# Performance work log

Hardware: AMD Instinct MI355X
Metric: run time of the kernel (lower is better)

The kernel has to match this reference:

```python
import jax, jax.numpy as jnp
import numpy as np

DIM = 128
KNN = 16
EPS = 1e-5


def knn_feature(coords, k):
    # coords: [B, K, D]; returns [B, K, k] nearest-neighbor indices (self excluded)
    inner = -2.0 * jnp.einsum('bid,bjd->bij', coords, coords)
    xx = jnp.sum(coords * coords, axis=-1, keepdims=True)  # [B,K,1]
    dist = xx + jnp.swapaxes(xx, 1, 2) + inner  # [B,K,K]
    K = coords.shape[1]
    diag = jnp.eye(K, dtype=bool)[None]
    dist = jnp.where(diag, 1e9, dist)
    _, idx = jax.lax.top_k(-dist, k)  # smallest distances
    return idx


def setup_inputs() -> dict:
    key = jax.random.key(0)
    ks = jax.random.split(key, 10)
    B, K, C = 8, 4096, DIM
    s1 = 1.0 / np.sqrt(2 * C)
    s2 = 1.0 / np.sqrt(C)
    return {
        'x': jax.random.normal(ks[0], (B, K, C), jnp.float32),
        'pos_embed': jax.random.normal(ks[1], (B, K, C), jnp.float32),
        'rel_pos_coords': jax.random.normal(ks[2], (B, K, 3), jnp.float32),
        'gamma': jnp.ones((C,), jnp.float32),
        'beta': jnp.zeros((C,), jnp.float32),
        'W_a1': jax.random.normal(ks[3], (2 * C, C), jnp.float32) * s1,
        'b_a1': jnp.zeros((C,), jnp.float32),
        'W_a2': jax.random.normal(ks[4], (C, 1), jnp.float32) * s2,
        'b_a2': jnp.zeros((1,), jnp.float32),
        'W_f1': jax.random.normal(ks[5], (2 * C, C), jnp.float32) * s1,
        'b_f1': jnp.zeros((C,), jnp.float32),
    }


def reference(x, pos_embed, rel_pos_coords, gamma, beta, W_a1, b_a1, W_a2, b_a2, W_f1, b_f1):
    B, K, C = x.shape
    k_eff = min(KNN, K - 1)
    # Pre-norm LayerNorm + positional embedding
    mu = jnp.mean(x, axis=-1, keepdims=True)
    var = jnp.mean((x - mu) ** 2, axis=-1, keepdims=True)
    x_norm = (x - mu) * jax.lax.rsqrt(var + EPS) * gamma + beta
    xp = x_norm + pos_embed  # [B,K,C]

    idx = knn_feature(rel_pos_coords, k_eff)  # [B,K,k]
    neighbor_feat = jax.vmap(lambda f, i: f[i])(xp, idx)  # [B,K,k,C]
    self_feat = jnp.broadcast_to(xp[:, :, None, :], neighbor_feat.shape)

    attn_in = jnp.concatenate([self_feat, neighbor_feat], axis=-1)  # [B,K,k,2C]
    h = jax.nn.leaky_relu(attn_in @ W_a1 + b_a1, 0.2)
    logits = h @ W_a2 + b_a2  # [B,K,k,1]
    attn = jax.nn.softmax(logits, axis=2)

    feat_in = jnp.concatenate([self_feat, neighbor_feat - self_feat], axis=-1)
    transformed = jax.nn.leaky_relu(feat_in @ W_f1 + b_f1, 0.2)  # [B,K,k,C]

    agg = jnp.sum(attn * transformed, axis=2)  # [B,K,C]
    # DropPath in eval mode is identity
    return agg
```

## Files before the change

kernel.cpp:

```cpp
#include <hip/hip_runtime.h>

#define B_ 8
#define K_ 4096
#define C_ 128
#define KN 16

typedef __attribute__((ext_vector_type(8))) short bf16x8;
typedef __attribute__((ext_vector_type(4))) float f32x4;

__device__ __forceinline__ unsigned short f2bf(float f) {
  unsigned u = __float_as_uint(f);
  unsigned r = (u + 0x7FFFu + ((u >> 16) & 1u)) >> 16;
  return (unsigned short)r;
}
__device__ __forceinline__ float bf2f(unsigned short s) {
  return __uint_as_float(((unsigned)s) << 16);
}

__device__ __forceinline__ float dist_exact(float4 q, float4 c) {
  float dot = __fadd_rn(__fadd_rn(__fmul_rn(q.x, c.x), __fmul_rn(q.y, c.y)),
                        __fmul_rn(q.z, c.z));
  return __fadd_rn(__fadd_rn(q.w, c.w), __fmul_rn(-2.0f, dot));
}
__device__ __forceinline__ float escr2(float qx2, float qy2, float qz2,
                                       float4 c) {
  return fmaf(-qx2, c.x, fmaf(-qy2, c.y, fmaf(-qz2, c.z, c.w)));
}

__global__ __launch_bounds__(256) void k_pre(
    const float* __restrict__ x, const float* __restrict__ pos,
    const float* __restrict__ gamma, const float* __restrict__ beta,
    const float* __restrict__ Wa1, const float* __restrict__ Wf1,
    const float* __restrict__ coords, unsigned short* __restrict__ A,
    unsigned short* __restrict__ WT, float4* __restrict__ cc4) {
  int blk = blockIdx.x;
  if (blk < 8192) {
    int wave = threadIdx.x >> 6;
    int lane = threadIdx.x & 63;
    size_t row = (size_t)blk * 4 + wave;
    const float2* xr = (const float2*)(x + row * C_);
    const float2* pr = (const float2*)(pos + row * C_);
    float2 a = xr[lane];
    float s = a.x + a.y;
#pragma unroll
    for (int o = 1; o < 64; o <<= 1) s += __shfl_xor(s, o);
    float mu = s * (1.0f / 128.0f);
    float dx = a.x - mu, dy = a.y - mu;
    float v = dx * dx + dy * dy;
#pragma unroll
    for (int o = 1; o < 64; o <<= 1) v += __shfl_xor(v, o);
    float rstd = rsqrtf(v * (1.0f / 128.0f) + 1e-5f);
    float2 gm = ((const float2*)gamma)[lane];
    float2 bt = ((const float2*)beta)[lane];
    float2 pp = pr[lane];
    float o0 = dx * rstd * gm.x + bt.x + pp.x;
    float o1 = dy * rstd * gm.y + bt.y + pp.y;
    ushort2 o = make_ushort2(f2bf(o0), f2bf(o1));
    *(ushort2*)(A + row * C_ + 2 * lane) = o;
  } else if (blk < 8320) {
    int i = (blk - 8192) * 256 + threadIdx.x;
    float px = coords[i * 3], py = coords[i * 3 + 1], pz = coords[i * 3 + 2];
    float w = __fadd_rn(__fadd_rn(__fmul_rn(px, px), __fmul_rn(py, py)),
                        __fmul_rn(pz, pz));
    cc4[i] = make_float4(px, py, pz, w);
  } else {
    int i = (blk - 8320) * 256 + threadIdx.x;
    int q = i >> 7;
    int r = i & 127;
    float v;
    if (q < 128)
      v = Wa1[r * 128 + q];
    else if (q < 256)
      v = Wf1[r * 128 + (q - 128)] - Wf1[(128 + r) * 128 + (q - 128)];
    else {
      int c = (q - 256) >> 1;
      if (((q - 256) & 1) == 0)
        v = Wa1[(128 + r) * 128 + c];
      else
        v = Wf1[(128 + r) * 128 + c];
    }
    WT[i] = f2bf(v);
  }
}

__global__ __launch_bounds__(256, 8) void k_knn(const float4* __restrict__ cc4,
                                                int* __restrict__ idx) {
  __shared__ unsigned cbuf[4][4][64];
  __shared__ unsigned scnt[4][4];
  int wave = threadIdx.x >> 6, lane = threadIdx.x & 63;
  int gw = blockIdx.x * 4 + wave;
  int b = gw >> 10;
  int qbase = (gw & 1023) * 4;
  const float4* cb = cc4 + (size_t)b * K_;
  if (lane < 4) scnt[wave][lane] = 0u;
  __asm__ volatile("s_waitcnt lgkmcnt(0)" ::: "memory");
  float4 Q[4];
  float qx2[4], qy2[4], qz2[4];
#pragma unroll
  for (int qq = 0; qq < 4; ++qq) {
    Q[qq] = cb[qbase + qq];
    qx2[qq] = 2.0f * Q[qq].x;
    qy2[qq] = 2.0f * Q[qq].y;
    qz2[qq] = 2.0f * Q[qq].z;
  }

  float m0 = 1e30f, m1 = 1e30f, m2 = 1e30f, m3 = 1e30f;
#pragma unroll 8
  for (int it = 0; it < 48; ++it) {
    float4 c = cb[(it << 6) + lane];
    m0 = fminf(m0, escr2(qx2[0], qy2[0], qz2[0], c));
    m1 = fminf(m1, escr2(qx2[1], qy2[1], qz2[1], c));
    m2 = fminf(m2, escr2(qx2[2], qy2[2], qz2[2], c));
    m3 = fminf(m3, escr2(qx2[3], qy2[3], qz2[3], c));
  }
  float ub[4];
  float mv[4] = {m0, m1, m2, m3};
#pragma unroll
  for (int qq = 0; qq < 4; ++qq) {
    float v = mv[qq];
#pragma unroll
    for (int k = 2; k <= 64; k <<= 1) {
#pragma unroll
      for (int jj = k >> 1; jj >= 1; jj >>= 1) {
        float o = __shfl_xor(v, jj);
        bool amHigh = (lane & jj) != 0;
        bool up = (lane & k) != 0;
        bool gt = v > o;
        bool take = (amHigh ? !gt : gt) ^ up;
        v = take ? o : v;
      }
    }
    ub[qq] = __shfl(v, 16) + 1e-3f;
  }

#pragma unroll 4
  for (int it = 0; it < 64; ++it) {
    int j = (it << 6) + lane;
    float4 c = cb[j];
#pragma unroll
    for (int qq = 0; qq < 4; ++qq) {
      float e = escr2(qx2[qq], qy2[qq], qz2[qq], c);
      if (e <= ub[qq]) {
        unsigned pos = atomicAdd(&scnt[wave][qq], 1u);
        if (pos < 64u) cbuf[wave][qq][pos] = (unsigned)j;
      }
    }
  }
  __asm__ volatile("s_waitcnt lgkmcnt(0)" ::: "memory");

#pragma unroll
  for (int qq = 0; qq < 4; ++qq) {
    unsigned m = scnt[wave][qq];
    m = m < 64u ? m : 64u;
    bool valid = lane < (int)m;
    unsigned ji = valid ? cbuf[wave][qq][lane] : 0u;
    if (valid && ji == (unsigned)(qbase + qq)) valid = false;
    float4 c = cb[ji];
    float dC = valid ? dist_exact(Q[qq], c) : 1e30f;
    int iC = valid ? (int)ji : 0x7fffffff;
#define SORT_STAGE(KV)                                              \
  {                                                                 \
    const int k = (KV);                                             \
    for (int jj = k >> 1; jj >= 1; jj >>= 1) {                      \
      float od = __shfl_xor(dC, jj);                                \
      int oi = __shfl_xor(iC, jj);                                  \
      bool amHigh = (lane & jj) != 0;                               \
      bool up = (lane & k) != 0;                                    \
      bool gt = (dC > od) || (dC == od && iC > oi);                 \
      bool take = (amHigh ? !gt : gt) ^ up;                         \
      dC = take ? od : dC;                                          \
      iC = take ? oi : iC;                                          \
    }                                                               \
  }
    if (m <= 32u) {
      SORT_STAGE(2) SORT_STAGE(4) SORT_STAGE(8) SORT_STAGE(16) SORT_STAGE(32)
    } else {
      SORT_STAGE(2) SORT_STAGE(4) SORT_STAGE(8) SORT_STAGE(16) SORT_STAGE(32)
      SORT_STAGE(64)
    }
#undef SORT_STAGE
    if (lane < KN)
      idx[((size_t)b * K_ + (qbase + qq)) * KN + lane] = iC;
  }
}

__global__ __launch_bounds__(256) void k_gemm_mfma(
    const unsigned short* __restrict__ A, const unsigned short* __restrict__ BT,
    unsigned short* __restrict__ SN) {
  __shared__ char lB[32768];
  int bb = blockIdx.x & 7;
  int rest = blockIdx.x >> 3;
  int mbl = rest >> 2, nb = rest & 3;
  int m0 = bb * 4096 + mbl * 128, n0 = nb * 128;
  int t = threadIdx.x;
  {
    const char* src = (const char*)(BT + (size_t)n0 * 128);
#pragma unroll
    for (int i = 0; i < 8; ++i) {
      int byte = (t + i * 256) * 16;
      int n = byte >> 8;
      int sb = byte ^ ((n & 7) << 4);
      *(float4*)(lB + sb) = *(const float4*)(src + byte);
    }
  }
  __syncthreads();
  int wave = t >> 6, lane = t & 63;
  int wr = wave >> 1, wc = wave & 1;
  int lm = lane & 15, lk = lane >> 4;
  f32x4 z = {0.f, 0.f, 0.f, 0.f};
  f32x4 acc00 = z, acc01 = z, acc02 = z, acc03 = z;
  f32x4 acc10 = z, acc11 = z, acc12 = z, acc13 = z;
  f32x4 acc20 = z, acc21 = z, acc22 = z, acc23 = z;
  f32x4 acc30 = z, acc31 = z, acc32 = z, acc33 = z;
  const char* abase =
      (const char*)A + (size_t)(m0 + wr * 64 + lm) * 256 + lk * 16;
#pragma unroll
  for (int ks = 0; ks < 4; ++ks) {
    bf16x8 af[4], bfr[4];
#pragma unroll
    for (int mt = 0; mt < 4; ++mt)
      af[mt] = *(const bf16x8*)(abase + (size_t)mt * 4096 + ks * 64);
#pragma unroll
    for (int nt = 0; nt < 4; ++nt) {
      int n_local = wc * 64 + nt * 16 + lm;
      int byte = n_local * 256 + ks * 64 + lk * 16;
      byte ^= (n_local & 7) << 4;
      bfr[nt] = *(const bf16x8*)(lB + byte);
    }
    acc00 = __builtin_amdgcn_mfma_f32_16x16x32_bf16(af[0], bfr[0], acc00, 0, 0, 0);
    acc01 = __builtin_amdgcn_mfma_f32_16x16x32_bf16(af[0], bfr[1], acc01, 0, 0, 0);
    acc02 = __builtin_amdgcn_mfma_f32_16x16x32_bf16(af[0], bfr[2], acc02, 0, 0, 0);
    acc03 = __builtin_amdgcn_mfma_f32_16x16x32_bf16(af[0], bfr[3], acc03, 0, 0, 0);
    acc10 = __builtin_amdgcn_mfma_f32_16x16x32_bf16(af[1], bfr[0], acc10, 0, 0, 0);
    acc11 = __builtin_amdgcn_mfma_f32_16x16x32_bf16(af[1], bfr[1], acc11, 0, 0, 0);
    acc12 = __builtin_amdgcn_mfma_f32_16x16x32_bf16(af[1], bfr[2], acc12, 0, 0, 0);
    acc13 = __builtin_amdgcn_mfma_f32_16x16x32_bf16(af[1], bfr[3], acc13, 0, 0, 0);
    acc20 = __builtin_amdgcn_mfma_f32_16x16x32_bf16(af[2], bfr[0], acc20, 0, 0, 0);
    acc21 = __builtin_amdgcn_mfma_f32_16x16x32_bf16(af[2], bfr[1], acc21, 0, 0, 0);
    acc22 = __builtin_amdgcn_mfma_f32_16x16x32_bf16(af[2], bfr[2], acc22, 0, 0, 0);
    acc23 = __builtin_amdgcn_mfma_f32_16x16x32_bf16(af[2], bfr[3], acc23, 0, 0, 0);
    acc30 = __builtin_amdgcn_mfma_f32_16x16x32_bf16(af[3], bfr[0], acc30, 0, 0, 0);
    acc31 = __builtin_amdgcn_mfma_f32_16x16x32_bf16(af[3], bfr[1], acc31, 0, 0, 0);
    acc32 = __builtin_amdgcn_mfma_f32_16x16x32_bf16(af[3], bfr[2], acc32, 0, 0, 0);
    acc33 = __builtin_amdgcn_mfma_f32_16x16x32_bf16(af[3], bfr[3], acc33, 0, 0, 0);
  }
  f32x4 accs[4][4] = {{acc00, acc01, acc02, acc03},
                      {acc10, acc11, acc12, acc13},
                      {acc20, acc21, acc22, acc23},
                      {acc30, acc31, acc32, acc33}};
#pragma unroll
  for (int mt = 0; mt < 4; ++mt) {
#pragma unroll
    for (int nt = 0; nt < 4; ++nt) {
#pragma unroll
      for (int r = 0; r < 4; ++r) {
        int row = m0 + wr * 64 + mt * 16 + lk * 4 + r;
        int col = n0 + wc * 64 + nt * 16 + lm;
        SN[(size_t)row * 512 + col] = f2bf(accs[mt][nt][r]);
      }
    }
  }
}

__global__ __launch_bounds__(256) void k_attn(
    const unsigned short* __restrict__ SN, const int* __restrict__ idx,
    const float* __restrict__ b_a1, const float* __restrict__ b_f1,
    const float* __restrict__ W_a2, const float* __restrict__ b_a2,
    float* __restrict__ out) {
  int wave = threadIdx.x >> 6, lane = threadIdx.x & 63;
  int g = lane >> 4, r = lane & 15;
  int b = blockIdx.x & 7;
  int w = blockIdx.x >> 3;
  size_t gpt = (size_t)b * K_ + w * 4 + wave;
  const unsigned short* sr = SN + gpt * 512;
  bf16x8 sa8 = *(const bf16x8*)(sr + 8 * r);
  bf16x8 sf8 = *(const bf16x8*)(sr + 128 + 8 * r);
  float4 bav0 = *(const float4*)(b_a1 + 8 * r);
  float4 bav1 = *(const float4*)(b_a1 + 8 * r + 4);
  float4 bfv0 = *(const float4*)(b_f1 + 8 * r);
  float4 bfv1 = *(const float4*)(b_f1 + 8 * r + 4);
  float4 w2v0 = *(const float4*)(W_a2 + 8 * r);
  float4 w2v1 = *(const float4*)(W_a2 + 8 * r + 4);
  float sab[8], sfb[8], w2v[8];
  {
    float bav[8] = {bav0.x, bav0.y, bav0.z, bav0.w, bav1.x, bav1.y, bav1.z, bav1.w};
    float bfv[8] = {bfv0.x, bfv0.y, bfv0.z, bfv0.w, bfv1.x, bfv1.y, bfv1.z, bfv1.w};
    float wv[8] = {w2v0.x, w2v0.y, w2v0.z, w2v0.w, w2v1.x, w2v1.y, w2v1.z, w2v1.w};
#pragma unroll
    for (int i = 0; i < 8; ++i) {
      sab[i] = bf2f((unsigned short)sa8[i]) + bav[i];
      sfb[i] = bf2f((unsigned short)sf8[i]) + bfv[i];
      w2v[i] = wv[i];
    }
  }
  float ba2v = b_a2[0];
  int nv = 0;
  if (lane < 16) nv = idx[gpt * 16 + lane];
  float lgl[4];
  float tsv[4][8];
#pragma unroll
  for (int round = 0; round < 4; ++round) {
    int n = __shfl(nv, round * 4 + g);
    const unsigned short* nr =
        SN + ((size_t)b * K_ + n) * 512 + 256 + 16 * r;
    bf16x8 u0 = *(const bf16x8*)(nr);
    bf16x8 u1 = *(const bf16x8*)(nr + 8);
    float dot = 0.0f;
#pragma unroll
    for (int i = 0; i < 4; ++i) {
      float h = sab[i] + bf2f((unsigned short)u0[2 * i]);
      h = h >= 0.0f ? h : 0.2f * h;
      float tv = sfb[i] + bf2f((unsigned short)u0[2 * i + 1]);
      tv = tv >= 0.0f ? tv : 0.2f * tv;
      dot = fmaf(h, w2v[i], dot);
      tsv[round][i] = tv;
    }
#pragma unroll
    for (int i = 0; i < 4; ++i) {
      float h = sab[4 + i] + bf2f((unsigned short)u1[2 * i]);
      h = h >= 0.0f ? h : 0.2f * h;
      float tv = sfb[4 + i] + bf2f((unsigned short)u1[2 * i + 1]);
      tv = tv >= 0.0f ? tv : 0.2f * tv;
      dot = fmaf(h, w2v[4 + i], dot);
      tsv[round][4 + i] = tv;
    }
#pragma unroll
    for (int o = 1; o < 16; o <<= 1) dot += __shfl_xor(dot, o);
    lgl[round] = dot + ba2v;
  }
  float mx = fmaxf(fmaxf(lgl[0], lgl[1]), fmaxf(lgl[2], lgl[3]));
  mx = fmaxf(mx, __shfl_xor(mx, 16));
  mx = fmaxf(mx, __shfl_xor(mx, 32));
  float e[4];
  float s = 0.0f;
#pragma unroll
  for (int round = 0; round < 4; ++round) {
    e[round] = expf(lgl[round] - mx);
    s += e[round];
  }
  s += __shfl_xor(s, 16);
  s += __shfl_xor(s, 32);
  float inv = 1.0f / s;
  float o8[8] = {0, 0, 0, 0, 0, 0, 0, 0};
#pragma unroll
  for (int round = 0; round < 4; ++round) {
    float a = e[round] * inv;
#pragma unroll
    for (int i = 0; i < 8; ++i) o8[i] = fmaf(a, tsv[round][i], o8[i]);
  }
#pragma unroll
  for (int i = 0; i < 8; ++i) {
    o8[i] += __shfl_xor(o8[i], 16);
    o8[i] += __shfl_xor(o8[i], 32);
  }
  if (g == 0) {
    float* op = out + gpt * 128 + 8 * r;
    *(float4*)op = make_float4(o8[0], o8[1], o8[2], o8[3]);
    *(float4*)(op + 4) = make_float4(o8[4], o8[5], o8[6], o8[7]);
  }
}

extern "C" void kernel_launch(void* const* d_in, const int* in_sizes, int n_in,
                              void* d_out, int out_size, void* d_ws,
                              size_t ws_size, hipStream_t stream) {
  const float* x = (const float*)d_in[0];
  const float* pos = (const float*)d_in[1];
  const float* coords = (const float*)d_in[2];
  const float* gamma = (const float*)d_in[3];
  const float* beta = (const float*)d_in[4];
  const float* Wa1 = (const float*)d_in[5];
  const float* ba1 = (const float*)d_in[6];
  const float* Wa2 = (const float*)d_in[7];
  const float* ba2 = (const float*)d_in[8];
  const float* Wf1 = (const float*)d_in[9];
  const float* bf1 = (const float*)d_in[10];
  float* out = (float*)d_out;

  char* ws = (char*)d_ws;
  unsigned short* A = (unsigned short*)ws;
  unsigned short* SN = (unsigned short*)(ws + (size_t)16 * 1024 * 1024);
  unsigned short* WT = (unsigned short*)(ws + (size_t)80 * 1024 * 1024);
  int* idx = (int*)(ws + (size_t)80 * 1024 * 1024 + 512 * 1024);
  float4* cc4 = (float4*)(ws + (size_t)80 * 1024 * 1024 + 2560 * 1024);

  k_pre<<<8576, 256, 0, stream>>>(x, pos, gamma, beta, Wa1, Wf1, coords, A, WT,
                                  cc4);
  k_knn<<<2048, 256, 0, stream>>>(cc4, idx);
  k_gemm_mfma<<<1024, 256, 0, stream>>>(A, WT, SN);
  k_attn<<<8192, 256, 0, stream>>>(SN, idx, ba1, bf1, Wa2, ba2, out);
}
```

Before: 114.5 us.

## Vectorize LayerNorm rows, stage GEMM output through LDS, reduce KNN unroll

```diff
diff --git a/kernel.cpp b/kernel.cpp
--- a/kernel.cpp
+++ b/kernel.cpp
@@ -34,37 +34,38 @@
     const float* __restrict__ coords, unsigned short* __restrict__ A,
     unsigned short* __restrict__ WT, float4* __restrict__ cc4) {
   int blk = blockIdx.x;
-  if (blk < 8192) {
+  if (blk < 4096) {
     int wave = threadIdx.x >> 6;
     int lane = threadIdx.x & 63;
-    size_t row = (size_t)blk * 4 + wave;
-    const float2* xr = (const float2*)(x + row * C_);
-    const float2* pr = (const float2*)(pos + row * C_);
-    float2 a = xr[lane];
-    float s = a.x + a.y;
-#pragma unroll
-    for (int o = 1; o < 64; o <<= 1) s += __shfl_xor(s, o);
+    int l32 = lane & 31;
+    size_t row = (size_t)blk * 8 + wave * 2 + (lane >> 5);
+    float4 a = ((const float4*)(x + row * C_))[l32];
+    float s = (a.x + a.y) + (a.z + a.w);
+#pragma unroll
+    for (int o = 1; o < 32; o <<= 1) s += __shfl_xor(s, o);
     float mu = s * (1.0f / 128.0f);
-    float dx = a.x - mu, dy = a.y - mu;
-    float v = dx * dx + dy * dy;
-#pragma unroll
-    for (int o = 1; o < 64; o <<= 1) v += __shfl_xor(v, o);
+    float d0 = a.x - mu, d1 = a.y - mu, d2 = a.z - mu, d3 = a.w - mu;
+    float v = (d0 * d0 + d1 * d1) + (d2 * d2 + d3 * d3);
+#pragma unroll
+    for (int o = 1; o < 32; o <<= 1) v += __shfl_xor(v, o);
     float rstd = rsqrtf(v * (1.0f / 128.0f) + 1e-5f);
-    float2 gm = ((const float2*)gamma)[lane];
-    float2 bt = ((const float2*)beta)[lane];
-    float2 pp = pr[lane];
-    float o0 = dx * rstd * gm.x + bt.x + pp.x;
-    float o1 = dy * rstd * gm.y + bt.y + pp.y;
-    ushort2 o = make_ushort2(f2bf(o0), f2bf(o1));
-    *(ushort2*)(A + row * C_ + 2 * lane) = o;
-  } else if (blk < 8320) {
-    int i = (blk - 8192) * 256 + threadIdx.x;
+    float4 gm = ((const float4*)gamma)[l32];
+    float4 bt = ((const float4*)beta)[l32];
+    float4 pp = ((const float4*)(pos + row * C_))[l32];
+    float o0 = d0 * rstd * gm.x + bt.x + pp.x;
+    float o1 = d1 * rstd * gm.y + bt.y + pp.y;
+    float o2 = d2 * rstd * gm.z + bt.z + pp.z;
+    float o3 = d3 * rstd * gm.w + bt.w + pp.w;
+    ushort4 o = make_ushort4(f2bf(o0), f2bf(o1), f2bf(o2), f2bf(o3));
+    *(ushort4*)(A + row * C_ + 4 * l32) = o;
+  } else if (blk < 4224) {
+    int i = (blk - 4096) * 256 + threadIdx.x;
     float px = coords[i * 3], py = coords[i * 3 + 1], pz = coords[i * 3 + 2];
     float w = __fadd_rn(__fadd_rn(__fmul_rn(px, px), __fmul_rn(py, py)),
                         __fmul_rn(pz, pz));
     cc4[i] = make_float4(px, py, pz, w);
   } else {
-    int i = (blk - 8320) * 256 + threadIdx.x;
+    int i = (blk - 4224) * 256 + threadIdx.x;
     int q = i >> 7;
     int r = i & 127;
     float v;
@@ -105,7 +106,7 @@
   }
 
   float m0 = 1e30f, m1 = 1e30f, m2 = 1e30f, m3 = 1e30f;
-#pragma unroll 8
+#pragma unroll 4
   for (int it = 0; it < 48; ++it) {
     float4 c = cb[(it << 6) + lane];
     m0 = fminf(m0, escr2(qx2[0], qy2[0], qz2[0], c));
@@ -133,7 +134,7 @@
     ub[qq] = __shfl(v, 16) + 1e-3f;
   }
 
-#pragma unroll 4
+#pragma unroll 2
   for (int it = 0; it < 64; ++it) {
     int j = (it << 6) + lane;
     float4 c = cb[j];
@@ -248,16 +249,29 @@
                       {acc10, acc11, acc12, acc13},
                       {acc20, acc21, acc22, acc23},
                       {acc30, acc31, acc32, acc33}};
+  __syncthreads();
+  unsigned short* lC = (unsigned short*)lB;
 #pragma unroll
   for (int mt = 0; mt < 4; ++mt) {
 #pragma unroll
     for (int nt = 0; nt < 4; ++nt) {
 #pragma unroll
       for (int r = 0; r < 4; ++r) {
-        int row = m0 + wr * 64 + mt * 16 + lk * 4 + r;
-        int col = n0 + wc * 64 + nt * 16 + lm;
-        SN[(size_t)row * 512 + col] = f2bf(accs[mt][nt][r]);
+        int row = wr * 64 + mt * 16 + lk * 4 + r;
+        int col = wc * 64 + nt * 16 + lm;
+        lC[row * 128 + col] = f2bf(accs[mt][nt][r]);
       }
+    }
+  }
+  __syncthreads();
+  {
+    unsigned short* dst = SN + (size_t)m0 * 512 + n0;
+#pragma unroll
+    for (int i = 0; i < 8; ++i) {
+      int e = (t + i * 256) * 8;
+      int row = e >> 7;
+      int col = e & 127;
+      *(f32x4*)(dst + (size_t)row * 512 + col) = *(const f32x4*)(lC + e);
     }
   }
 }
@@ -383,7 +397,7 @@
   int* idx = (int*)(ws + (size_t)80 * 1024 * 1024 + 512 * 1024);
   float4* cc4 = (float4*)(ws + (size_t)80 * 1024 * 1024 + 2560 * 1024);
 
-  k_pre<<<8576, 256, 0, stream>>>(x, pos, gamma, beta, Wa1, Wf1, coords, A, WT,
+  k_pre<<<4480, 256, 0, stream>>>(x, pos, gamma, beta, Wa1, Wf1, coords, A, WT,
                                   cc4);
   k_knn<<<2048, 256, 0, stream>>>(cc4, idx);
   k_gemm_mfma<<<1024, 256, 0, stream>>>(A, WT, SN);
```

Result: faster. 111.2 us (-2.9%).
